# Performance work log

Hardware: AMD Instinct MI355X
Metric: run time of the kernel (lower is better)

## Reference

```python
import jax, jax.numpy as jnp
import numpy as np

H = 2048          # hidden_size
NH = 16           # num_attention_heads
NKV = 4           # num_key_value_heads
HD = 128          # head_dim
B, S = 2, 2048
EPS = 1e-6


def _rms_norm(x, w):
    # RMSNorm over last dim (head_dim)
    var = jnp.mean(jnp.square(x), axis=-1, keepdims=True)
    return x * jax.lax.rsqrt(var + EPS) * w


def _rotate_half(x):
    x1, x2 = jnp.split(x, 2, axis=-1)
    return jnp.concatenate([-x2, x1], axis=-1)


def _apply_rope(x, cos, sin):
    # x: [b, s, h, d]; cos/sin: [s, d]
    c = cos[None, :, None, :]
    s = sin[None, :, None, :]
    return x * c + _rotate_half(x) * s


def setup_inputs() -> dict:
    key = jax.random.key(0)
    ks = jax.random.split(key, 12)
    hidden_states = jax.random.normal(ks[0], (B, S, H), dtype=jnp.float32)
    # RoPE tables (base 10000, full head_dim)
    inv_freq = 1.0 / (10000.0 ** (np.arange(0, HD, 2, dtype=np.float32) / HD))
    t = np.arange(S, dtype=np.float32)
    freqs = np.outer(t, inv_freq)                      # [S, HD/2]
    emb = np.concatenate([freqs, freqs], axis=-1)      # [S, HD]
    cos = jnp.asarray(np.cos(emb), dtype=jnp.float32)
    sin = jnp.asarray(np.sin(emb), dtype=jnp.float32)
    scale = 0.02
    Wq = jax.random.normal(ks[1], (H, NH * HD), jnp.float32) * scale
    bq = jax.random.normal(ks[2], (NH * HD,), jnp.float32) * scale
    Wk = jax.random.normal(ks[3], (H, NKV * HD), jnp.float32) * scale
    bk = jax.random.normal(ks[4], (NKV * HD,), jnp.float32) * scale
    Wv = jax.random.normal(ks[5], (H, NKV * HD), jnp.float32) * scale
    bv = jax.random.normal(ks[6], (NKV * HD,), jnp.float32) * scale
    Wo = jax.random.normal(ks[7], (NH * HD, H), jnp.float32) * scale
    bo = jax.random.normal(ks[8], (H,), jnp.float32) * scale
    q_norm_w = jnp.ones((HD,), jnp.float32)
    k_norm_w = jnp.ones((HD,), jnp.float32)
    cu_seqlens = jnp.array([0, S, 2 * S], dtype=jnp.int32)
    max_s = S
    return {"hidden_states": hidden_states, "cos": cos, "sin": sin,
            "Wq": Wq, "bq": bq, "Wk": Wk, "bk": bk, "Wv": Wv, "bv": bv,
            "Wo": Wo, "bo": bo, "q_norm_w": q_norm_w, "k_norm_w": k_norm_w,
            "cu_seqlens": cu_seqlens, "max_s": max_s}


def reference(hidden_states, cos, sin, Wq, bq, Wk, bk, Wv, bv, Wo, bo,
              q_norm_w, k_norm_w, cu_seqlens, max_s):
    b, s, _ = hidden_states.shape
    q = (hidden_states @ Wq + bq).reshape(b, s, NH, HD)
    k = (hidden_states @ Wk + bk).reshape(b, s, NKV, HD)
    v = (hidden_states @ Wv + bv).reshape(b, s, NKV, HD)
    q = _rms_norm(q, q_norm_w)
    k = _rms_norm(k, k_norm_w)
    q = _apply_rope(q, cos, sin)
    k = _apply_rope(k, cos, sin)
    # GQA: repeat_interleave kv heads to match query heads
    n_rep = NH // NKV
    k = jnp.repeat(k, n_rep, axis=2)   # [b, s, NH, HD]
    v = jnp.repeat(v, n_rep, axis=2)
    scale = 1.0 / jnp.sqrt(jnp.float32(HD))
    # scores: [b, h, s_q, s_k]
    scores = jnp.einsum('bqhd,bkhd->bhqk', q, k) * scale
    neg = jnp.finfo(scores.dtype).min
    causal = jnp.triu(jnp.ones((s, s), dtype=bool), k=1)
    scores = scores + jnp.where(causal, neg, 0.0)[None, None]
    weights = jax.nn.softmax(scores, axis=-1)
    attn = jnp.einsum('bhqk,bkhd->bqhd', weights, v).reshape(b, s, NH * HD)
    return attn @ Wo + bo
```

## Files before the change

kernel.cpp:

```cpp
#include <hip/hip_runtime.h>
#include <math.h>

#define H 2048
#define NH 16
#define NKV 4
#define HD 128
#define BB 2
#define SS 2048
#define NT (BB*SS)
#define NQK (NH*HD)
#define NKVD (NKV*HD)
#define NQKV (NQK + 2*NKVD)
#define EPSV 1e-6f
#define SM_SCALE 0.08838834764831845f
#define LOG2E 1.4426950408889634f

using s8v = __attribute__((ext_vector_type(8))) short;
using s4v = __attribute__((ext_vector_type(4))) short;
using f4v = __attribute__((ext_vector_type(4))) float;

typedef unsigned int __attribute__((address_space(1))) u32_g;
typedef unsigned int __attribute__((address_space(3))) u32_l;

__device__ inline float bf2f(short s){ unsigned u = ((unsigned)(unsigned short)s) << 16; return __builtin_bit_cast(float, u); }
__device__ inline short f2bf(float f){ unsigned u = __builtin_bit_cast(unsigned, f); u += 0x7FFF + ((u>>16)&1); return (short)(u>>16); }

__device__ inline f4v mfma16(s8v a, s8v b, f4v c){
    return __builtin_amdgcn_mfma_f32_16x16x32_bf16(a, b, c, 0, 0, 0);
}

__device__ inline void gl_lds16(const short* g, short* l){
    __builtin_amdgcn_global_load_lds((const u32_g*)g, (u32_l*)l, 16, 0, 0);
}


__global__ void cvt_f32_bf16(const float* __restrict__ in, short* __restrict__ out, int n4){
    int i = blockIdx.x*blockDim.x + threadIdx.x;
    int stride = gridDim.x*blockDim.x;
    for (; i < n4; i += stride){
        float4 v = reinterpret_cast<const float4*>(in)[i];
        s4v o = { f2bf(v.x), f2bf(v.y), f2bf(v.z), f2bf(v.w) };
        reinterpret_cast<s4v*>(out)[i] = o;
    }
}

__global__ __launch_bounds__(256) void transpose_cvt(const float* __restrict__ src, short* __restrict__ dst,
                                                     int R, int C){
    __shared__ short t[64][72];
    const int tid = threadIdx.x;
    const int r0 = blockIdx.y*64, c0 = blockIdx.x*64;
    #pragma unroll
    for (int it = 0; it < 4; ++it){
        int ch = tid + it*256;
        int row = ch >> 4, c4 = (ch & 15) * 4;
        float4 v = *reinterpret_cast<const float4*>(src + (size_t)(r0+row)*C + c0 + c4);
        t[row][c4+0] = f2bf(v.x); t[row][c4+1] = f2bf(v.y);
        t[row][c4+2] = f2bf(v.z); t[row][c4+3] = f2bf(v.w);
    }
    __syncthreads();
    #pragma unroll
    for (int it = 0; it < 4; ++it){
        int ch = tid + it*256;
        int cc = ch >> 4, r4 = (ch & 15) * 4;
        s4v o = { t[r4+0][cc], t[r4+1][cc], t[r4+2][cc], t[r4+3][cc] };
        *reinterpret_cast<s4v*>(dst + (size_t)(c0+cc)*R + r0 + r4) = o;
    }
}

__global__ void concat_b(const float* __restrict__ bq, const float* __restrict__ bk,
                         const float* __restrict__ bv, float* __restrict__ Bc){
    int i = blockIdx.x*blockDim.x + threadIdx.x;
    if (i < NQKV)
        Bc[i] = (i < NQK) ? bq[i] : (i < NQK+NKVD ? bk[i-NQK] : bv[i-NQK-NKVD]);
}


template<int OUT_F32>
__global__ __launch_bounds__(256) void gemm_bt(const short* __restrict__ A, const short* __restrict__ BT,
                                               const float* __restrict__ bias, void* __restrict__ Cout,
                                               int M, int N, int K){
    __shared__ short As[2][4096];
    __shared__ short Bs[2][4096];
    const int tid  = threadIdx.x;
    const int lane = tid & 63;
    const int wv   = tid >> 6;
    const int f    = lane & 15;
    const int g    = lane >> 4;

    int lin = blockIdx.y * gridDim.x + blockIdx.x;
    int cpx = (gridDim.x * gridDim.y) >> 3;
    int sw  = (lin & 7) * cpx + (lin >> 3);
    const int m0 = (sw / gridDim.x) * 128;
    const int n0 = (sw % gridDim.x) * 128;

    const int mb   = (wv & 1) * 64;
    const int nb   = (wv >> 1) * 64;
    f4v acc[4][4] = {};

    const short* Abase = A  + (size_t)m0*K;
    const short* Bbase = BT + (size_t)n0*K;
    const int srow = (lane >> 2);
    const int scol = (lane & 3) * 8;

    auto STAGE = [&](int buf, int k0){
        #pragma unroll
        for (int c = 0; c < 2; ++c){
            int issue = wv + c*4;
            int row = issue*16 + srow;
            gl_lds16(Abase + (size_t)row*K + k0 + scol, &As[buf][issue*512]);
            gl_lds16(Bbase + (size_t)row*K + k0 + scol, &Bs[buf][issue*512]);
        }
    };

    STAGE(0, 0);
    asm volatile("s_waitcnt vmcnt(0)" ::: "memory");
    __syncthreads();
    int cur = 0;
    for (int k0 = 0; k0 < K; k0 += 32){
        if (k0 + 32 < K) STAGE(cur^1, k0 + 32);
        s8v a[4], bfr[4];
        #pragma unroll
        for (int i = 0; i < 4; ++i) a[i]   = *reinterpret_cast<const s8v*>(&As[cur][(mb + i*16 + f)*32 + g*8]);
        #pragma unroll
        for (int j = 0; j < 4; ++j) bfr[j] = *reinterpret_cast<const s8v*>(&Bs[cur][(nb + j*16 + f)*32 + g*8]);
        #pragma unroll
        for (int i = 0; i < 4; ++i)
            #pragma unroll
            for (int j = 0; j < 4; ++j)
                acc[i][j] = mfma16(a[i], bfr[j], acc[i][j]);
        asm volatile("s_waitcnt vmcnt(0)" ::: "memory");
        __syncthreads();
        cur ^= 1;
    }

    #pragma unroll
    for (int i = 0; i < 4; ++i){
        #pragma unroll
        for (int j = 0; j < 4; ++j){
            int col = n0 + nb + j*16 + f;
            float bvv = bias ? bias[col] : 0.f;
            #pragma unroll
            for (int r = 0; r < 4; ++r){
                int row = m0 + mb + i*16 + g*4 + r;
                float vv = acc[i][j][r] + bvv;
                if (OUT_F32) reinterpret_cast<float*>(Cout)[(size_t)row*N + col] = vv;
                else         reinterpret_cast<short*>(Cout)[(size_t)row*N + col] = f2bf(vv);
            }
        }
    }
}


__global__ __launch_bounds__(256) void norm_rope(short* __restrict__ qkv, const float* __restrict__ cosb,
                                                 const float* __restrict__ sinb, const float* __restrict__ qw,
                                                 const float* __restrict__ kw){
    int row  = blockIdx.x * 4 + (threadIdx.x >> 6);
    int lane = threadIdx.x & 63;
    const int QROWS = NT * NH;
    short* ptr; const float* w; float outscale; int token;
    if (row < QROWS){
        token = row >> 4; int h = row & 15;
        ptr = qkv + (size_t)token*NQKV + h*HD; w = qw; outscale = SM_SCALE * LOG2E;
    } else {
        int rr = row - QROWS;
        token = rr >> 2; int h = rr & 3;
        ptr = qkv + (size_t)token*NQKV + NQK + h*HD; w = kw; outscale = 1.f;
    }
    int s = token & (SS-1);
    float x1 = bf2f(ptr[lane]), x2 = bf2f(ptr[lane+64]);
    float ssq = x1*x1 + x2*x2;
    #pragma unroll
    for (int off = 32; off; off >>= 1) ssq += __shfl_xor(ssq, off, 64);
    float inv = rsqrtf(ssq * (1.f/128.f) + EPSV);
    float n1 = x1 * inv * w[lane];
    float n2 = x2 * inv * w[lane+64];
    float c1 = cosb[s*HD + lane], c2 = cosb[s*HD + lane + 64];
    float s1 = sinb[s*HD + lane], s2 = sinb[s*HD + lane + 64];
    float o1 = (n1*c1 - n2*s1) * outscale;
    float o2 = (n2*c2 + n1*s2) * outscale;
    ptr[lane]    = f2bf(o1);
    ptr[lane+64] = f2bf(o2);
}


__global__ __launch_bounds__(256) void vtrans(const short* __restrict__ qkv, short* __restrict__ Vt){
    __shared__ short t[64][72];
    const int tid = threadIdx.x;
    const int s0 = blockIdx.x*64, c0 = blockIdx.y*64, b = blockIdx.z;
    #pragma unroll
    for (int it = 0; it < 2; ++it){
        int ch = tid + it*256;
        int row = ch >> 3, col = (ch & 7)*8;
        s8v v = *reinterpret_cast<const s8v*>(qkv + (size_t)(b*SS + s0 + row)*NQKV + NQK + NKVD + c0 + col);
        *reinterpret_cast<s8v*>(&t[row][col]) = v;
    }
    __syncthreads();
    #pragma unroll
    for (int it = 0; it < 2; ++it){
        int ch = tid + it*256;
        int cc = ch >> 3, sc = (ch & 7)*8;
        s8v o;
        #pragma unroll
        for (int j = 0; j < 8; ++j) o[j] = t[sc + j][cc];
        *reinterpret_cast<s8v*>(Vt + (size_t)(b*NKVD + c0 + cc)*SS + s0 + sc) = o;
    }
}


__global__ __launch_bounds__(512, 4) void attn_fwd(const short* __restrict__ qkv, const short* __restrict__ Vt,
                                                   short* __restrict__ attn){
    __shared__ short Ks[2][8192];
    __shared__ short Vs[2][8192];
    __shared__ short Ps[8][1024];
    const int tid  = threadIdx.x;
    const int lane = tid & 63;
    const int w    = tid >> 6;
    const int f    = lane & 15;
    const int g    = lane >> 4;
    const int bx   = blockIdx.x;
    const int qt   = 63 - (bx >> 3);
    const int kvh  = bx & 3;
    const int b    = (bx >> 2) & 1;
    const int h    = kvh*4 + (w >> 1);
    const int half = w & 1;
    const int q0   = qt * 32;
    const int qrow0 = q0 + half*16;
    char* Pb = (char*)Ps[w];

    auto STAGEK = [&](int buf, int kv0){
        #pragma unroll
        for (int c = 0; c < 2; ++c){
            int issue = w + c*8;
            int row = issue*4 + g;
            int col16 = f ^ (row & 7);
            gl_lds16(qkv + (size_t)(b*SS + kv0 + row)*NQKV + NQK + kvh*HD + col16*8,
                     &Ks[buf][issue*512]);
        }
    };
    auto STAGEV = [&](int buf, int kv0){
        #pragma unroll
        for (int c = 0; c < 2; ++c){
            int issue = w + c*8;
            int row = issue*8 + (lane >> 3);
            int col16 = (lane & 7) ^ (row & 7);
            gl_lds16(Vt + (size_t)(b*NKVD + kvh*HD + row)*SS + kv0 + col16*8,
                     &Vs[buf][issue*512]);
        }
    };

    s8v qa[4];
    #pragma unroll
    for (int dc = 0; dc < 4; ++dc)
        qa[dc] = *reinterpret_cast<const s8v*>(
            qkv + (size_t)(b*SS + qrow0 + f)*NQKV + h*HD + dc*32 + g*8);

    f4v acc[8] = {};
    float m_[4], lp_[4];
    #pragma unroll
    for (int r = 0; r < 4; ++r){ m_[r] = -3e38f; lp_[r] = 0.f; }

    const int nt = (q0 + 32 + 63) >> 6;
    STAGEK(0, 0);
    STAGEV(0, 0);
    asm volatile("s_waitcnt vmcnt(0)" ::: "memory");
    __builtin_amdgcn_sched_barrier(0);
    __builtin_amdgcn_s_barrier();
    int cur = 0;

    for (int t = 0; t < nt; ++t){
        const int kv0 = t*64;
        if (t + 1 < nt){ STAGEK(cur^1, kv0 + 64); STAGEV(cur^1, kv0 + 64); }

        f4v sf[4] = {};
        __builtin_amdgcn_s_setprio(1);
        #pragma unroll
        for (int kh = 0; kh < 4; ++kh){
            const int krow = kh*16 + f;
            #pragma unroll
            for (int dc = 0; dc < 4; ++dc){
                s8v kb = *reinterpret_cast<const s8v*>(
                    (const char*)Ks[cur] + krow*256 + ((dc*64 + g*16) ^ ((krow & 7) << 4)));
                sf[kh] = mfma16(qa[dc], kb, sf[kh]);
            }
        }
        __builtin_amdgcn_s_setprio(0);

        if (kv0 + 63 > qrow0){
            #pragma unroll
            for (int kh = 0; kh < 4; ++kh){
                int key = kv0 + kh*16 + f;
                #pragma unroll
                for (int r = 0; r < 4; ++r){
                    int qrow = qrow0 + g*4 + r;
                    if (key > qrow) sf[kh][r] = -3e38f;
                }
            }
        }

        float mloc[4];
        bool need = false;
        #pragma unroll
        for (int r = 0; r < 4; ++r){
            mloc[r] = fmaxf(fmaxf(sf[0][r], sf[1][r]), fmaxf(sf[2][r], sf[3][r]));
            need = need || (mloc[r] > m_[r] + 11.0f);
        }
        if (__any(need)){
            #pragma unroll
            for (int r = 0; r < 4; ++r){
                float mx = mloc[r];
                #pragma unroll
                for (int off = 8; off; off >>= 1) mx = fmaxf(mx, __shfl_xor(mx, off, 16));
                float mn = fmaxf(m_[r], mx);
                float al = __builtin_amdgcn_exp2f(m_[r] - mn);
                m_[r] = mn;
                lp_[r] *= al;
                #pragma unroll
                for (int df = 0; df < 8; ++df) acc[df][r] *= al;
            }
        }

        #pragma unroll
        for (int r = 0; r < 4; ++r){
            const int prow = g*4 + r;
            #pragma unroll
            for (int kh = 0; kh < 4; ++kh){
                float p = __builtin_amdgcn_exp2f(sf[kh][r] - m_[r]);
                short pb = f2bf(p);
                lp_[r] += bf2f(pb);
                *(short*)(Pb + prow*128 + ((unsigned)((kh*16 + f)*2) ^ ((prow & 7) << 4))) = pb;
            }
        }

        __builtin_amdgcn_s_setprio(1);
        #pragma unroll
        for (int ks = 0; ks < 2; ++ks){
            s8v pa = *reinterpret_cast<const s8v*>(
                Pb + f*128 + ((ks*64 + g*16) ^ ((f & 7) << 4)));
            #pragma unroll
            for (int df = 0; df < 8; ++df){
                const int vrow = df*16 + f;
                s8v vb = *reinterpret_cast<const s8v*>(
                    (const char*)Vs[cur] + vrow*128 + ((ks*64 + g*16) ^ ((vrow & 7) << 4)));
                acc[df] = mfma16(pa, vb, acc[df]);
            }
        }
        __builtin_amdgcn_s_setprio(0);

        asm volatile("s_waitcnt vmcnt(0)" ::: "memory");
        __builtin_amdgcn_sched_barrier(0);
        __builtin_amdgcn_s_barrier();
        cur ^= 1;
    }

    #pragma unroll
    for (int r = 0; r < 4; ++r){
        float l = lp_[r];
        #pragma unroll
        for (int off = 8; off; off >>= 1) l += __shfl_xor(l, off, 16);
        int qrow = qrow0 + g*4 + r;
        float inv = 1.f / l;
        short* ob = attn + (size_t)(b*SS + qrow)*NQK + h*HD;
        #pragma unroll
        for (int df = 0; df < 8; ++df)
            ob[df*16 + f] = f2bf(acc[df][r] * inv);
    }
}


extern "C" void kernel_launch(void* const* d_in, const int* in_sizes, int n_in,
                              void* d_out, int out_size, void* d_ws, size_t ws_size,
                              hipStream_t stream){
    (void)in_sizes; (void)n_in; (void)out_size; (void)ws_size;
    const float* hs   = (const float*)d_in[0];
    const float* cosb = (const float*)d_in[1];
    const float* sinb = (const float*)d_in[2];
    const float* Wq   = (const float*)d_in[3];
    const float* bq   = (const float*)d_in[4];
    const float* Wk   = (const float*)d_in[5];
    const float* bk   = (const float*)d_in[6];
    const float* Wv   = (const float*)d_in[7];
    const float* bv   = (const float*)d_in[8];
    const float* Wo   = (const float*)d_in[9];
    const float* bo   = (const float*)d_in[10];
    const float* qw   = (const float*)d_in[11];
    const float* kw   = (const float*)d_in[12];
    float* out = (float*)d_out;
    char* ws = (char*)d_ws;

    size_t off = 0;
    auto alloc = [&](size_t bytes){ size_t o = off; off += (bytes + 255) & ~(size_t)255; return o; };
    short* Xb    = (short*)(ws + alloc((size_t)NT*H*2));
    short* Wct   = (short*)(ws + alloc((size_t)NQKV*H*2));
    float* Bc    = (float*)(ws + alloc((size_t)NQKV*4));
    short* QKV   = (short*)(ws + alloc((size_t)NT*NQKV*2));
    short* Vt    = (short*)(ws + alloc((size_t)BB*NKVD*SS*2 + 4096));
    short* attnb = (short*)(ws + alloc((size_t)NT*NQK*2));
    short* WoT   = (short*)(ws + alloc((size_t)H*NQK*2));

    cvt_f32_bf16<<<2048, 256, 0, stream>>>(hs, Xb, NT*H/4);
    transpose_cvt<<<dim3(NQK/64,  H/64), 256, 0, stream>>>(Wq, Wct,                        H, NQK);
    transpose_cvt<<<dim3(NKVD/64, H/64), 256, 0, stream>>>(Wk, Wct + (size_t)NQK*H,        H, NKVD);
    transpose_cvt<<<dim3(NKVD/64, H/64), 256, 0, stream>>>(Wv, Wct + (size_t)(NQK+NKVD)*H, H, NKVD);
    transpose_cvt<<<dim3(H/64,  NQK/64), 256, 0, stream>>>(Wo, WoT,                        NQK, H);
    concat_b<<<3, 1024, 0, stream>>>(bq, bk, bv, Bc);

    gemm_bt<0><<<dim3(NQKV/128, NT/128), 256, 0, stream>>>(Xb, Wct, Bc, QKV, NT, NQKV, H);
    norm_rope<<<(NT*(NH+NKV))/4, 256, 0, stream>>>(QKV, cosb, sinb, qw, kw);
    vtrans<<<dim3(SS/64, NKVD/64, BB), 256, 0, stream>>>(QKV, Vt);
    attn_fwd<<<512, 512, 0, stream>>>(QKV, Vt, attnb);
    gemm_bt<1><<<dim3(H/128, NT/128), 256, 0, stream>>>(attnb, WoT, bo, out, NT, H, NQK);
}
```

Before: 349.8 us.

## Replace GEMM with 8-wave 256-row tiled kernel using swizzled LDS and phased MFMA

Replaces the 128x128, 4-wave, K=32 GEMM with an 8-wave kernel using 256xBN tiles and K=64 stages. It XOR-swizzles the LDS layout to avoid bank conflicts and interleaves global-to-LDS prefetch with four MFMA phases, using s_setprio. The aim is more reuse per LDS load and better overlap of memory and compute in the QKV and output projections. Larger tiles mean fewer blocks: the output GEMM gets 16x16=256 blocks, which may underfill 256 CUs at 2 blocks each. The larger LDS footprint and register count can also limit occupancy.

```diff
diff --git a/kernel.cpp b/kernel.cpp
--- a/kernel.cpp
+++ b/kernel.cpp
@@ -75,74 +75,122 @@
 }
 
 
-template<int OUT_F32>
-__global__ __launch_bounds__(256) void gemm_bt(const short* __restrict__ A, const short* __restrict__ BT,
-                                               const float* __restrict__ bias, void* __restrict__ Cout,
-                                               int M, int N, int K){
-    __shared__ short As[2][4096];
-    __shared__ short Bs[2][4096];
+template<int BN, int OUT_F32>
+__global__ __launch_bounds__(512, 2) void gemm8(const short* __restrict__ A, const short* __restrict__ BT,
+                                                const float* __restrict__ bias, void* __restrict__ Cout,
+                                                int M, int N, int K){
+    constexpr int WN  = BN/4;
+    constexpr int NF  = WN/16;
+    constexpr int NFH = NF/2;
+    constexpr int BCH = BN/64;
+    __shared__ short As[2][256*64];
+    __shared__ short Bs[2][BN*64];
     const int tid  = threadIdx.x;
     const int lane = tid & 63;
-    const int wv   = tid >> 6;
+    const int w    = tid >> 6;
     const int f    = lane & 15;
     const int g    = lane >> 4;
+    const int wm   = w >> 2;
+    const int wn   = w & 3;
 
     int lin = blockIdx.y * gridDim.x + blockIdx.x;
     int cpx = (gridDim.x * gridDim.y) >> 3;
     int sw  = (lin & 7) * cpx + (lin >> 3);
-    const int m0 = (sw / gridDim.x) * 128;
-    const int n0 = (sw % gridDim.x) * 128;
-
-    const int mb   = (wv & 1) * 64;
-    const int nb   = (wv >> 1) * 64;
-    f4v acc[4][4] = {};
-
-    const short* Abase = A  + (size_t)m0*K;
-    const short* Bbase = BT + (size_t)n0*K;
-    const int srow = (lane >> 2);
-    const int scol = (lane & 3) * 8;
-
-    auto STAGE = [&](int buf, int k0){
-        #pragma unroll
-        for (int c = 0; c < 2; ++c){
-            int issue = wv + c*4;
-            int row = issue*16 + srow;
-            gl_lds16(Abase + (size_t)row*K + k0 + scol, &As[buf][issue*512]);
-            gl_lds16(Bbase + (size_t)row*K + k0 + scol, &Bs[buf][issue*512]);
+    const int m0 = (sw / gridDim.x) * 256;
+    const int n0 = (sw % gridDim.x) * BN;
+
+    const short* Ab = A  + (size_t)m0*K;
+    const short* Bb = BT + (size_t)n0*K;
+
+    f4v acc[8][NF] = {};
+
+    auto STAGE_A = [&](int buf, int k0){
+        #pragma unroll
+        for (int c = 0; c < 4; ++c){
+            int j = c*8 + w;
+            int row = j*8 + (lane >> 3);
+            int slot = (lane & 7) ^ (row & 7);
+            gl_lds16(Ab + (size_t)row*K + k0 + slot*8, &As[buf][j*512]);
         }
     };
-
-    STAGE(0, 0);
+    auto STAGE_B = [&](int buf, int k0){
+        #pragma unroll
+        for (int c = 0; c < BCH; ++c){
+            int j = c*8 + w;
+            int row = j*8 + (lane >> 3);
+            int slot = (lane & 7) ^ (row & 7);
+            gl_lds16(Bb + (size_t)row*K + k0 + slot*8, &Bs[buf][j*512]);
+        }
+    };
+
+    auto PH = [&](int buf, int qm, int qn){
+        s8v a[4][2], b[NFH][2];
+        #pragma unroll
+        for (int mi = 0; mi < 4; ++mi){
+            int row = wm*128 + (qm*4 + mi)*16 + f;
+            #pragma unroll
+            for (int ks = 0; ks < 2; ++ks)
+                a[mi][ks] = *reinterpret_cast<const s8v*>(
+                    &As[buf][row*64 + ((ks*4 + g) ^ (row & 7))*8]);
+        }
+        #pragma unroll
+        for (int ni = 0; ni < NFH; ++ni){
+            int row = wn*WN + (qn*NFH + ni)*16 + f;
+            #pragma unroll
+            for (int ks = 0; ks < 2; ++ks)
+                b[ni][ks] = *reinterpret_cast<const s8v*>(
+                    &Bs[buf][row*64 + ((ks*4 + g) ^ (row & 7))*8]);
+        }
+        __builtin_amdgcn_s_barrier();
+        __builtin_amdgcn_s_setprio(1);
+        #pragma unroll
+        for (int mi = 0; mi < 4; ++mi)
+            #pragma unroll
+            for (int ni = 0; ni < NFH; ++ni)
+                #pragma unroll
+                for (int ks = 0; ks < 2; ++ks)
+                    acc[qm*4 + mi][qn*NFH + ni] =
+                        mfma16(a[mi][ks], b[ni][ks], acc[qm*4 + mi][qn*NFH + ni]);
+        __builtin_amdgcn_s_setprio(0);
+    };
+
+    const int NITER = K >> 7;
+    STAGE_A(0, 0); STAGE_B(0, 0);
     asm volatile("s_waitcnt vmcnt(0)" ::: "memory");
-    __syncthreads();
-    int cur = 0;
-    for (int k0 = 0; k0 < K; k0 += 32){
-        if (k0 + 32 < K) STAGE(cur^1, k0 + 32);
-        s8v a[4], bfr[4];
-        #pragma unroll
-        for (int i = 0; i < 4; ++i) a[i]   = *reinterpret_cast<const s8v*>(&As[cur][(mb + i*16 + f)*32 + g*8]);
-        #pragma unroll
-        for (int j = 0; j < 4; ++j) bfr[j] = *reinterpret_cast<const s8v*>(&Bs[cur][(nb + j*16 + f)*32 + g*8]);
-        #pragma unroll
-        for (int i = 0; i < 4; ++i)
-            #pragma unroll
-            for (int j = 0; j < 4; ++j)
-                acc[i][j] = mfma16(a[i], bfr[j], acc[i][j]);
+    __builtin_amdgcn_sched_barrier(0);
+    __builtin_amdgcn_s_barrier();
+
+    for (int it = 0; it < NITER; ++it){
+        const int k0 = it*128;
+        STAGE_A(1, k0 + 64);  PH(0, 0, 0);
+        STAGE_B(1, k0 + 64);  PH(0, 0, 1);
+        PH(0, 1, 0);
+        PH(0, 1, 1);
         asm volatile("s_waitcnt vmcnt(0)" ::: "memory");
-        __syncthreads();
-        cur ^= 1;
-    }
-
-    #pragma unroll
-    for (int i = 0; i < 4; ++i){
-        #pragma unroll
-        for (int j = 0; j < 4; ++j){
-            int col = n0 + nb + j*16 + f;
+        __builtin_amdgcn_sched_barrier(0);
+        __builtin_amdgcn_s_barrier();
+        const bool pf = (it + 1 < NITER);
+        if (pf) STAGE_A(0, k0 + 128);
+        PH(1, 0, 0);
+        if (pf) STAGE_B(0, k0 + 128);
+        PH(1, 0, 1);
+        PH(1, 1, 0);
+        PH(1, 1, 1);
+        asm volatile("s_waitcnt vmcnt(0)" ::: "memory");
+        __builtin_amdgcn_sched_barrier(0);
+        __builtin_amdgcn_s_barrier();
+    }
+
+    #pragma unroll
+    for (int mf = 0; mf < 8; ++mf){
+        #pragma unroll
+        for (int nf = 0; nf < NF; ++nf){
+            int col = n0 + wn*WN + nf*16 + f;
             float bvv = bias ? bias[col] : 0.f;
             #pragma unroll
             for (int r = 0; r < 4; ++r){
-                int row = m0 + mb + i*16 + g*4 + r;
-                float vv = acc[i][j][r] + bvv;
+                int row = m0 + wm*128 + mf*16 + g*4 + r;
+                float vv = acc[mf][nf][r] + bvv;
                 if (OUT_F32) reinterpret_cast<float*>(Cout)[(size_t)row*N + col] = vv;
                 else         reinterpret_cast<short*>(Cout)[(size_t)row*N + col] = f2bf(vv);
             }
@@ -404,9 +452,9 @@
     transpose_cvt<<<dim3(H/64,  NQK/64), 256, 0, stream>>>(Wo, WoT,                        NQK, H);
     concat_b<<<3, 1024, 0, stream>>>(bq, bk, bv, Bc);
 
-    gemm_bt<0><<<dim3(NQKV/128, NT/128), 256, 0, stream>>>(Xb, Wct, Bc, QKV, NT, NQKV, H);
+    gemm8<256,0><<<dim3(NQKV/256, NT/256), 512, 0, stream>>>(Xb, Wct, Bc, QKV, NT, NQKV, H);
     norm_rope<<<(NT*(NH+NKV))/4, 256, 0, stream>>>(QKV, cosb, sinb, qw, kw);
     vtrans<<<dim3(SS/64, NKVD/64, BB), 256, 0, stream>>>(QKV, Vt);
     attn_fwd<<<512, 512, 0, stream>>>(QKV, Vt, attnb);
-    gemm_bt<1><<<dim3(H/128, NT/128), 256, 0, stream>>>(attnb, WoT, bo, out, NT, H, NQK);
-}
+    gemm8<128,1><<<dim3(H/128, NT/256), 512, 0, stream>>>(attnb, WoT, bo, out, NT, H, NQK);
+}
```

After: 361.8 us. 1.03x slower.
